# Performance work log

Hardware: AMD Instinct MI355X
Metric: run time of the kernel (lower is better)

Reference implementation:

```python
import jax, jax.numpy as jnp
import numpy as np

K = 24  # number of clusters (all ids in [0,K) assumed present per image)
DELTA_VAR = 1.0
DELTA_DIST = 2.0
VAR_W = 1.0
DIST_W = 1.0
REG_W = 1.0


def setup_inputs() -> dict:
    key = jax.random.key(0)
    k1, k2 = jax.random.split(key)
    data = jax.random.normal(k1, (4, 16, 512, 1024), dtype=jnp.float32)
    labels = jax.random.randint(k2, (4, 512, 1024), 0, K, dtype=jnp.int32)
    return {"data": data, "labels": labels}


def reference(data, labels):
    B, D, H, Wd = data.shape
    N = H * Wd
    # [B, N, D] points, [B*N] global segment ids (batch-offset cluster ids)
    X = jnp.transpose(data.reshape(B, D, N), (0, 2, 1)).reshape(B * N, D)
    seg = (labels.reshape(B, N) + jnp.arange(B, dtype=labels.dtype)[:, None] * K).reshape(-1)

    # per-cluster sums and counts -> centers  [B*K, D]
    sums = jax.ops.segment_sum(X, seg, num_segments=B * K)
    counts = jax.ops.segment_sum(jnp.ones((B * N,), X.dtype), seg, num_segments=B * K)
    centers_flat = sums / counts[:, None]
    centers = centers_flat.reshape(B, K, D)
    counts_bk = counts.reshape(B, K)

    # variance term: per-point hinged distance to own cluster center
    c_per_point = centers_flat[seg]                      # [B*N, D]
    pt_dist = jnp.linalg.norm(X - c_per_point, axis=1)   # [B*N]
    hv = jnp.maximum(pt_dist - DELTA_VAR, 0.0) ** 2
    var_per_cluster = jax.ops.segment_sum(hv, seg, num_segments=B * K).reshape(B, K) / counts_bk
    var_sum = var_per_cluster.sum()

    # distance term: pairwise center distances (diagonal kept, as in original,
    # contributing a constant delta_dist**2 per cluster)
    diff = centers[:, :, None, :] - centers[:, None, :, :]     # [B, K, K, D]
    sq = jnp.sum(diff * diff, axis=-1)                         # [B, K, K]
    eye = jnp.eye(K, dtype=bool)[None]
    cdist = jnp.where(eye, 0.0, jnp.sqrt(jnp.where(eye, 1.0, sq)))
    hd = jnp.maximum(DELTA_DIST - cdist, 0.0) ** 2
    dist_sum = hd.sum() / (2.0 * K * (K - 1))

    # regularization: mean center norm per image, summed over batch
    reg_sum = jnp.linalg.norm(centers, axis=2).mean(axis=1).sum()

    loss = (VAR_W * var_sum + DIST_W * dist_sum + REG_W * reg_sum) / B
    return loss
```

## Files before the change

kernel.cpp:

```cpp
#include <hip/hip_runtime.h>
#include <math.h>

#define KC 24
constexpr int D = 16;
constexpr int B = 4;
constexpr int N = 512 * 1024;
constexpr float DELTA_VAR = 1.0f;
constexpr float DELTA_DIST = 2.0f;

constexpr int REP = 8;
constexpr int RS  = KC * 17;
constexpr int CS  = 33;
constexpr int TPB = 512;
constexpr int PTS = 8192;
constexpr int NBLK = (B * N) / PTS;
constexpr int SL = 8;
constexpr int RLDS = 4;
constexpr int RREG = 12;
constexpr int WS_FLOATS = SL * (B * KC * D) + SL * (B * KC) + 64;


__device__ __forceinline__ float gldf(const float* p) {
    return __hip_atomic_load(p, __ATOMIC_RELAXED, __HIP_MEMORY_SCOPE_AGENT);
}

__device__ __forceinline__ void gsync(int* cnt, int* gen) {
    __syncthreads();
    if (threadIdx.x == 0) {
        int g = __hip_atomic_load(gen, __ATOMIC_ACQUIRE, __HIP_MEMORY_SCOPE_AGENT);
        if (__hip_atomic_fetch_add(cnt, 1, __ATOMIC_ACQ_REL, __HIP_MEMORY_SCOPE_AGENT) == NBLK - 1) {
            __hip_atomic_store(cnt, 0, __ATOMIC_RELAXED, __HIP_MEMORY_SCOPE_AGENT);
            __hip_atomic_fetch_add(gen, 1, __ATOMIC_ACQ_REL, __HIP_MEMORY_SCOPE_AGENT);
        } else {
            for (int it = 0; it < (1 << 24); ++it) {
                if (__hip_atomic_load(gen, __ATOMIC_ACQUIRE, __HIP_MEMORY_SCOPE_AGENT) != g) break;
                __builtin_amdgcn_s_sleep(2);
            }
        }
    }
    __syncthreads();
}

#define KEEP4(f4) asm volatile("" : "+v"((f4).x), "+v"((f4).y), "+v"((f4).z), "+v"((f4).w))

__global__ __launch_bounds__(TPB) void k_fused(const float* __restrict__ data,
                                               const int* __restrict__ labels,
                                               float* __restrict__ ws,
                                               float* __restrict__ out) {
    __shared__ float s_sum[REP * RS];
    __shared__ float s_cnt[REP * CS];
    __shared__ __align__(16) float4 s_data4[RLDS][PTS / 4];
    __shared__ float s_c[KC * 17];
    __shared__ float s_ic[KC];
    __shared__ float s_red[8];

    float* g_sums = ws;
    float* g_cnt  = ws + SL * (B * KC * D);
    float* g_varp = g_cnt + SL * (B * KC);
    int*   bar    = (int*)(g_varp + 64);

    const int t = threadIdx.x;
    const int chunk = blockIdx.x * PTS;
    const int b = chunk >> 19;
    const float* base = data + (size_t)(b * D) * N + (chunk & (N - 1));

    int4 lab[4];
#pragma unroll
    for (int i = 0; i < 4; ++i)
        lab[i] = *(const int4*)(labels + chunk + (i * TPB + t) * 4);

    float4 tmp[2][4];
#pragma unroll
    for (int i = 0; i < 4; ++i)
        tmp[0][i] = *(const float4*)(base + (i * TPB + t) * 4);

    for (int i = t; i < REP * RS; i += TPB) s_sum[i] = 0.f;
    for (int i = t; i < REP * CS; i += TPB) s_cnt[i] = 0.f;
    __syncthreads();

    const int rbase = (t & 7) * RS;
    const int cbase = (t & 7) * CS;
#pragma unroll
    for (int i = 0; i < 4; ++i) {
        atomicAdd(&s_cnt[cbase + lab[i].x], 1.f);
        atomicAdd(&s_cnt[cbase + lab[i].y], 1.f);
        atomicAdd(&s_cnt[cbase + lab[i].z], 1.f);
        atomicAdd(&s_cnt[cbase + lab[i].w], 1.f);
    }

    float4 vr[RREG][4];
#pragma unroll
    for (int d = 0; d < D; ++d) {
        if (d + 1 < D) {
#pragma unroll
            for (int i = 0; i < 4; ++i) {
                float4 nx = *(const float4*)(base + (size_t)(d + 1) * N + (i * TPB + t) * 4);
                if (d + 1 < RLDS) tmp[(d + 1) & 1][i] = nx;
                else              vr[d + 1 - RLDS][i] = nx;
            }
        }
#pragma unroll
        for (int i = 0; i < 4; ++i) {
            const float4 c = (d < RLDS) ? tmp[d & 1][i] : vr[d - RLDS][i];
            if (d < RLDS) s_data4[d][i * TPB + t] = c;
            atomicAdd(&s_sum[rbase + lab[i].x * 17 + d], c.x);
            atomicAdd(&s_sum[rbase + lab[i].y * 17 + d], c.y);
            atomicAdd(&s_sum[rbase + lab[i].z * 17 + d], c.z);
            atomicAdd(&s_sum[rbase + lab[i].w * 17 + d], c.w);
        }
    }

#pragma unroll
    for (int d = 0; d < RREG; ++d)
#pragma unroll
        for (int i = 0; i < 4; ++i) KEEP4(vr[d][i]);

    __syncthreads();

    const int slice = blockIdx.x & (SL - 1);
    float* gs = g_sums + slice * (B * KC * D) + b * (KC * D);
    float* gc = g_cnt  + slice * (B * KC)     + b * KC;
    const int rot = (blockIdx.x * 131) & 255;
    for (int i = t; i < KC * D; i += TPB) {
        int j = (i + rot) % (KC * D);
        int c = j >> 4, dd = j & 15;
        float s = 0.f;
#pragma unroll
        for (int r = 0; r < REP; ++r) s += s_sum[r * RS + c * 17 + dd];
        atomicAdd(&gs[j], s);
    }
    if (t < KC) {
        float s = 0.f;
#pragma unroll
        for (int r = 0; r < REP; ++r) s += s_cnt[r * CS + t];
        atomicAdd(&gc[t], s);
    }

    gsync(bar, bar + 1);

    if (t < KC) {
        float cn = 0.f;
#pragma unroll
        for (int r = 0; r < SL; ++r) cn += gldf(&g_cnt[r * (B * KC) + b * KC + t]);
        s_ic[t] = 1.f / cn;
    }
    __syncthreads();
    for (int i = t; i < KC * D; i += TPB) {
        int c = i >> 4, dd = i & 15;
        float s = 0.f;
#pragma unroll
        for (int r = 0; r < SL; ++r) s += gldf(&g_sums[r * (B * KC * D) + b * (KC * D) + i]);
        s_c[c * 17 + dd] = s * s_ic[c];
    }
    __syncthreads();

    float ac[16];
#pragma unroll
    for (int i = 0; i < 16; ++i) ac[i] = 0.f;

#pragma unroll
    for (int p = 0; p < RLDS; ++p) {
        const int d = p;
#pragma unroll
        for (int i = 0; i < 4; ++i) {
            const float4 c = s_data4[p][i * TPB + t];
            float df;
            df = c.x - s_c[lab[i].x * 17 + d]; ac[i * 4 + 0] += df * df;
            df = c.y - s_c[lab[i].y * 17 + d]; ac[i * 4 + 1] += df * df;
            df = c.z - s_c[lab[i].z * 17 + d]; ac[i * 4 + 2] += df * df;
            df = c.w - s_c[lab[i].w * 17 + d]; ac[i * 4 + 3] += df * df;
        }
    }
#pragma unroll
    for (int rr = 0; rr < RREG; ++rr) {
        const int d = RLDS + rr;
#pragma unroll
        for (int i = 0; i < 4; ++i) {
            const float4 c = vr[rr][i];
            float df;
            df = c.x - s_c[lab[i].x * 17 + d]; ac[i * 4 + 0] += df * df;
            df = c.y - s_c[lab[i].y * 17 + d]; ac[i * 4 + 1] += df * df;
            df = c.z - s_c[lab[i].z * 17 + d]; ac[i * 4 + 2] += df * df;
            df = c.w - s_c[lab[i].w * 17 + d]; ac[i * 4 + 3] += df * df;
        }
    }

    float hsum = 0.f;
#pragma unroll
    for (int i = 0; i < 4; ++i) {
        float h;
        h = fmaxf(sqrtf(ac[i * 4 + 0]) - DELTA_VAR, 0.f); hsum += h * h * s_ic[lab[i].x];
        h = fmaxf(sqrtf(ac[i * 4 + 1]) - DELTA_VAR, 0.f); hsum += h * h * s_ic[lab[i].y];
        h = fmaxf(sqrtf(ac[i * 4 + 2]) - DELTA_VAR, 0.f); hsum += h * h * s_ic[lab[i].z];
        h = fmaxf(sqrtf(ac[i * 4 + 3]) - DELTA_VAR, 0.f); hsum += h * h * s_ic[lab[i].w];
    }
    for (int o = 32; o > 0; o >>= 1) hsum += __shfl_down(hsum, o, 64);
    if ((t & 63) == 0) s_red[t >> 6] = hsum;
    __syncthreads();
    if (t == 0) {
        float s = 0.f;
#pragma unroll
        for (int w = 0; w < 8; ++w) s += s_red[w];
        atomicAdd(&g_varp[blockIdx.x & 63], s);
    }

    gsync(bar, bar + 1);

    if (blockIdx.x != 0) return;

    float* s_cF = (float*)&s_data4[0][0];
    float acc = 0.f;
    if (t < B * KC) {
        float cnt = 0.f;
#pragma unroll
        for (int r = 0; r < SL; ++r) cnt += gldf(&g_cnt[r * (B * KC) + t]);
        float ns = 0.f;
        for (int dd = 0; dd < D; ++dd) {
            float s = 0.f;
#pragma unroll
            for (int r = 0; r < SL; ++r) s += gldf(&g_sums[r * (B * KC * D) + t * D + dd]);
            float c = s / cnt;
            s_cF[t * 17 + dd] = c;
            ns += c * c;
        }
        acc = sqrtf(ns) / (float)KC;
    }
    if (t < 64) acc += gldf(&g_varp[t]);
    __syncthreads();

    float dacc = 0.f;
    for (int idx = t; idx < B * KC * KC; idx += TPB) {
        int bb = idx / (KC * KC);
        int r = idx % (KC * KC);
        int i = r / KC, j = r % KC;
        float hd;
        if (i == j) {
            hd = DELTA_DIST * DELTA_DIST;
        } else {
            const float* ci = &s_cF[(bb * KC + i) * 17];
            const float* cj = &s_cF[(bb * KC + j) * 17];
            float sq = 0.f;
            for (int dd = 0; dd < D; ++dd) { float df = ci[dd] - cj[dd]; sq += df * df; }
            float hh = fmaxf(DELTA_DIST - sqrtf(sq), 0.f);
            hd = hh * hh;
        }
        dacc += hd;
    }
    float total = acc + dacc / (2.f * KC * (KC - 1));

    for (int o = 32; o > 0; o >>= 1) total += __shfl_down(total, o, 64);
    if ((t & 63) == 0) s_red[t >> 6] = total;
    __syncthreads();
    if (t == 0) {
        float s = 0.f;
#pragma unroll
        for (int w = 0; w < 8; ++w) s += s_red[w];
        out[0] = s / (float)B;
    }
}

extern "C" void kernel_launch(void* const* d_in, const int* in_sizes, int n_in,
                              void* d_out, int out_size, void* d_ws, size_t ws_size,
                              hipStream_t stream) {
    const float* data  = (const float*)d_in[0];
    const int* labels  = (const int*)d_in[1];
    float* ws          = (float*)d_ws;

    hipMemsetAsync(d_ws, 0, WS_FLOATS * sizeof(float) + 2 * sizeof(int), stream);
    k_fused<<<NBLK, TPB, 0, stream>>>(data, labels, ws, (float*)d_out);
}
```

Measured before the change: 398.6 us.

## Store point features as packed bf16 and use expanded-norm distance

Point features are truncated to bf16 and packed two per 32-bit word, half held in LDS and half in registers, instead of keeping fp32 copies. The distance to the center is computed as ||x||^2 - 2x·c + ||c||^2: ||x||^2 is accumulated in fp32 during the first pass and ||c||^2 once per cluster. Launch bounds now request two blocks per CU. The aim is lower register pressure and a cheaper second pass, at the cost of precision loss from bf16 truncation and cancellation in the expanded form.

```diff
diff --git a/kernel.cpp b/kernel.cpp
--- a/kernel.cpp
+++ b/kernel.cpp
@@ -15,8 +15,6 @@
 constexpr int PTS = 8192;
 constexpr int NBLK = (B * N) / PTS;
 constexpr int SL = 8;
-constexpr int RLDS = 4;
-constexpr int RREG = 12;
 constexpr int WS_FLOATS = SL * (B * KC * D) + SL * (B * KC) + 64;
 
 
@@ -41,17 +39,19 @@
     __syncthreads();
 }
 
-#define KEEP4(f4) asm volatile("" : "+v"((f4).x), "+v"((f4).y), "+v"((f4).z), "+v"((f4).w))
-
-__global__ __launch_bounds__(TPB) void k_fused(const float* __restrict__ data,
-                                               const int* __restrict__ labels,
-                                               float* __restrict__ ws,
-                                               float* __restrict__ out) {
+__device__ __forceinline__ float blo(unsigned u) { return __uint_as_float(u << 16); }
+__device__ __forceinline__ float bhi(unsigned u) { return __uint_as_float(u & 0xFFFF0000u); }
+
+__global__ __launch_bounds__(TPB, 2) void k_fused(const float* __restrict__ data,
+                                                  const int* __restrict__ labels,
+                                                  float* __restrict__ ws,
+                                                  float* __restrict__ out) {
     __shared__ float s_sum[REP * RS];
     __shared__ float s_cnt[REP * CS];
-    __shared__ __align__(16) float4 s_data4[RLDS][PTS / 4];
+    __shared__ uint2 s_xb[8][PTS / 4];
     __shared__ float s_c[KC * 17];
     __shared__ float s_ic[KC];
+    __shared__ float s_c2[KC];
     __shared__ float s_red[8];
 
     float* g_sums = ws;
@@ -69,10 +69,10 @@
     for (int i = 0; i < 4; ++i)
         lab[i] = *(const int4*)(labels + chunk + (i * TPB + t) * 4);
 
-    float4 tmp[2][4];
+    float4 va[4], vb[4];
 #pragma unroll
     for (int i = 0; i < 4; ++i)
-        tmp[0][i] = *(const float4*)(base + (i * TPB + t) * 4);
+        va[i] = *(const float4*)(base + (i * TPB + t) * 4);
 
     for (int i = t; i < REP * RS; i += TPB) s_sum[i] = 0.f;
     for (int i = t; i < REP * CS; i += TPB) s_cnt[i] = 0.f;
@@ -88,21 +88,31 @@
         atomicAdd(&s_cnt[cbase + lab[i].w], 1.f);
     }
 
-    float4 vr[RREG][4];
+    float r2[16];
+#pragma unroll
+    for (int p = 0; p < 16; ++p) r2[p] = 0.f;
+    unsigned xb[8][8];
+
 #pragma unroll
     for (int d = 0; d < D; ++d) {
         if (d + 1 < D) {
 #pragma unroll
             for (int i = 0; i < 4; ++i) {
                 float4 nx = *(const float4*)(base + (size_t)(d + 1) * N + (i * TPB + t) * 4);
-                if (d + 1 < RLDS) tmp[(d + 1) & 1][i] = nx;
-                else              vr[d + 1 - RLDS][i] = nx;
+                if ((d + 1) & 1) vb[i] = nx; else va[i] = nx;
             }
         }
 #pragma unroll
         for (int i = 0; i < 4; ++i) {
-            const float4 c = (d < RLDS) ? tmp[d & 1][i] : vr[d - RLDS][i];
-            if (d < RLDS) s_data4[d][i * TPB + t] = c;
+            const float4 c = (d & 1) ? vb[i] : va[i];
+            r2[i * 4 + 0] = fmaf(c.x, c.x, r2[i * 4 + 0]);
+            r2[i * 4 + 1] = fmaf(c.y, c.y, r2[i * 4 + 1]);
+            r2[i * 4 + 2] = fmaf(c.z, c.z, r2[i * 4 + 2]);
+            r2[i * 4 + 3] = fmaf(c.w, c.w, r2[i * 4 + 3]);
+            unsigned pxy = (__float_as_uint(c.y) & 0xFFFF0000u) | (__float_as_uint(c.x) >> 16);
+            unsigned pzw = (__float_as_uint(c.w) & 0xFFFF0000u) | (__float_as_uint(c.z) >> 16);
+            if (d < 8) s_xb[d][i * TPB + t] = make_uint2(pxy, pzw);
+            else       { xb[d - 8][i * 2 + 0] = pxy; xb[d - 8][i * 2 + 1] = pzw; }
             atomicAdd(&s_sum[rbase + lab[i].x * 17 + d], c.x);
             atomicAdd(&s_sum[rbase + lab[i].y * 17 + d], c.y);
             atomicAdd(&s_sum[rbase + lab[i].z * 17 + d], c.z);
@@ -111,9 +121,14 @@
     }
 
 #pragma unroll
-    for (int d = 0; d < RREG; ++d)
-#pragma unroll
-        for (int i = 0; i < 4; ++i) KEEP4(vr[d][i]);
+    for (int dd = 0; dd < 8; ++dd)
+#pragma unroll
+        for (int q = 0; q < 8; ++q) asm volatile("" : "+v"(xb[dd][q]));
+#pragma unroll
+    for (int p = 0; p < 16; ++p) asm volatile("" : "+v"(r2[p]));
+#pragma unroll
+    for (int i = 0; i < 4; ++i)
+        asm volatile("" : "+v"(lab[i].x), "+v"(lab[i].y), "+v"(lab[i].z), "+v"(lab[i].w));
 
     __syncthreads();
 
@@ -153,46 +168,46 @@
         s_c[c * 17 + dd] = s * s_ic[c];
     }
     __syncthreads();
-
-    float ac[16];
-#pragma unroll
-    for (int i = 0; i < 16; ++i) ac[i] = 0.f;
-
-#pragma unroll
-    for (int p = 0; p < RLDS; ++p) {
-        const int d = p;
-#pragma unroll
-        for (int i = 0; i < 4; ++i) {
-            const float4 c = s_data4[p][i * TPB + t];
-            float df;
-            df = c.x - s_c[lab[i].x * 17 + d]; ac[i * 4 + 0] += df * df;
-            df = c.y - s_c[lab[i].y * 17 + d]; ac[i * 4 + 1] += df * df;
-            df = c.z - s_c[lab[i].z * 17 + d]; ac[i * 4 + 2] += df * df;
-            df = c.w - s_c[lab[i].w * 17 + d]; ac[i * 4 + 3] += df * df;
-        }
-    }
-#pragma unroll
-    for (int rr = 0; rr < RREG; ++rr) {
-        const int d = RLDS + rr;
-#pragma unroll
-        for (int i = 0; i < 4; ++i) {
-            const float4 c = vr[rr][i];
-            float df;
-            df = c.x - s_c[lab[i].x * 17 + d]; ac[i * 4 + 0] += df * df;
-            df = c.y - s_c[lab[i].y * 17 + d]; ac[i * 4 + 1] += df * df;
-            df = c.z - s_c[lab[i].z * 17 + d]; ac[i * 4 + 2] += df * df;
-            df = c.w - s_c[lab[i].w * 17 + d]; ac[i * 4 + 3] += df * df;
-        }
-    }
+    if (t < KC) {
+        float q = 0.f;
+#pragma unroll
+        for (int dd = 0; dd < D; ++dd) q = fmaf(s_c[t * 17 + dd], s_c[t * 17 + dd], q);
+        s_c2[t] = q;
+    }
+    __syncthreads();
 
     float hsum = 0.f;
 #pragma unroll
     for (int i = 0; i < 4; ++i) {
-        float h;
-        h = fmaxf(sqrtf(ac[i * 4 + 0]) - DELTA_VAR, 0.f); hsum += h * h * s_ic[lab[i].x];
-        h = fmaxf(sqrtf(ac[i * 4 + 1]) - DELTA_VAR, 0.f); hsum += h * h * s_ic[lab[i].y];
-        h = fmaxf(sqrtf(ac[i * 4 + 2]) - DELTA_VAR, 0.f); hsum += h * h * s_ic[lab[i].z];
-        h = fmaxf(sqrtf(ac[i * 4 + 3]) - DELTA_VAR, 0.f); hsum += h * h * s_ic[lab[i].w];
+        const float* cx = &s_c[lab[i].x * 17];
+        const float* cy = &s_c[lab[i].y * 17];
+        const float* cz = &s_c[lab[i].z * 17];
+        const float* cw = &s_c[lab[i].w * 17];
+        float d0 = 0.f, d1 = 0.f, d2 = 0.f, d3 = 0.f;
+#pragma unroll
+        for (int d = 0; d < 8; ++d) {
+            uint2 u = s_xb[d][i * TPB + t];
+            d0 = fmaf(blo(u.x), cx[d], d0);
+            d1 = fmaf(bhi(u.x), cy[d], d1);
+            d2 = fmaf(blo(u.y), cz[d], d2);
+            d3 = fmaf(bhi(u.y), cw[d], d3);
+        }
+#pragma unroll
+        for (int d = 0; d < 8; ++d) {
+            d0 = fmaf(blo(xb[d][i * 2 + 0]), cx[8 + d], d0);
+            d1 = fmaf(bhi(xb[d][i * 2 + 0]), cy[8 + d], d1);
+            d2 = fmaf(blo(xb[d][i * 2 + 1]), cz[8 + d], d2);
+            d3 = fmaf(bhi(xb[d][i * 2 + 1]), cw[8 + d], d3);
+        }
+        float q, h;
+        q = fmaxf(fmaf(-2.f, d0, r2[i * 4 + 0]) + s_c2[lab[i].x], 0.f);
+        h = fmaxf(sqrtf(q) - DELTA_VAR, 0.f); hsum += h * h * s_ic[lab[i].x];
+        q = fmaxf(fmaf(-2.f, d1, r2[i * 4 + 1]) + s_c2[lab[i].y], 0.f);
+        h = fmaxf(sqrtf(q) - DELTA_VAR, 0.f); hsum += h * h * s_ic[lab[i].y];
+        q = fmaxf(fmaf(-2.f, d2, r2[i * 4 + 2]) + s_c2[lab[i].z], 0.f);
+        h = fmaxf(sqrtf(q) - DELTA_VAR, 0.f); hsum += h * h * s_ic[lab[i].z];
+        q = fmaxf(fmaf(-2.f, d3, r2[i * 4 + 3]) + s_c2[lab[i].w], 0.f);
+        h = fmaxf(sqrtf(q) - DELTA_VAR, 0.f); hsum += h * h * s_ic[lab[i].w];
     }
     for (int o = 32; o > 0; o >>= 1) hsum += __shfl_down(hsum, o, 64);
     if ((t & 63) == 0) s_red[t >> 6] = hsum;
@@ -208,7 +223,7 @@
 
     if (blockIdx.x != 0) return;
 
-    float* s_cF = (float*)&s_data4[0][0];
+    float* s_cF = (float*)&s_xb[0][0];
     float acc = 0.f;
     if (t < B * KC) {
         float cnt = 0.f;
```

Measured after the change: 387.6 us. 1.03x faster.
